# Optimization experiments

Hardware: AMD Instinct MI355X
Metric: run time of the kernel (lower is better)

## Reference

```python
import jax, jax.numpy as jnp
import numpy as np

N, F, D, H = 8192, 128, 128, 2
LEAKY_ALPHA = 0.3  # keras.layers.LeakyReLU default


def setup_inputs() -> dict:
    key = jax.random.key(0)
    ks = jax.random.split(key, 8)
    x = jax.random.normal(ks[0], (N, F), dtype=jnp.float32)
    # sparse-ish binary adjacency with self loops, stored dense (as the module does)
    adj = (jax.random.uniform(ks[1], (N, N)) < 0.01).astype(jnp.float32)
    adj = jnp.clip(adj + jnp.eye(N, dtype=jnp.float32), 0.0, 1.0)
    s = 1.0 / np.sqrt(F)
    Wmap = jax.random.normal(ks[2], (H, F, D), dtype=jnp.float32) * s
    a1_w = jax.random.normal(ks[3], (H, D), dtype=jnp.float32) * (1.0 / np.sqrt(D))
    a2_w = jax.random.normal(ks[4], (H, D), dtype=jnp.float32) * (1.0 / np.sqrt(D))
    a1_b = jnp.zeros((H,), dtype=jnp.float32)
    a2_b = jnp.zeros((H,), dtype=jnp.float32)
    kernel = jax.random.normal(ks[5], (H, F, D), dtype=jnp.float32) * s
    bias = jnp.zeros((H, N, D), dtype=jnp.float32)
    return {"x": x, "adj": adj, "Wmap": Wmap, "a1_w": a1_w, "a1_b": a1_b,
            "a2_w": a2_w, "a2_b": a2_b, "kernel": kernel, "bias": bias}


def reference(x, adj, Wmap, a1_w, a1_b, a2_w, a2_b, kernel, bias):
    # per-head Conv1D(k=1, no bias): node-wise linear map  [H, N, D]
    mapped = jnp.einsum('nf,hfd->hnd', x, Wmap)
    # per-head Conv1D(k=1) scalar scores  [H, N]
    sa1 = jnp.einsum('hnd,hd->hn', mapped, a1_w) + a1_b[:, None]
    sa2 = jnp.einsum('hnd,hd->hn', mapped, a2_w) + a2_b[:, None]
    # additive score masked multiplicatively by adjacency:  [H, N, N]
    w = adj[None, :, :] * sa1[:, :, None] + adj[None, :, :] * sa2[:, None, :]
    w = jnp.where(w >= 0, w, LEAKY_ALPHA * w)
    att = jax.nn.softmax(w, axis=-1)  # softmax over neighbors (incl. zeroed entries, as in source)
    value = jnp.einsum('nf,hfd->hnd', x, kernel)
    out = jnp.einsum('hnm,hmd->hnd', att, value) + bias  # [H, N, D]
    return out.mean(axis=0)  # attn_heads_reduction='average', linear activation
```

## Files before the change

kernel.cpp:

```cpp
#include <hip/hip_runtime.h>
#include <hip/hip_bf16.h>

#define NN 8192
#define FF 128
#define DD 128
#define HH 2
#define ALPHA 0.3f
#define MAXNNZ 1024

__global__ __launch_bounds__(256) void c_kernel(
    const float* __restrict__ Wmap, const float* __restrict__ a1w,
    const float* __restrict__ a2w, float* __restrict__ c1, float* __restrict__ c2) {
  int t = threadIdx.x;
  int h = t >> 7, f = t & 127;
  const float* wrow = Wmap + ((size_t)h * FF + f) * DD;
  const float* a1 = a1w + h * DD;
  const float* a2 = a2w + h * DD;
  float s1 = 0.f, s2 = 0.f;
  #pragma unroll 8
  for (int d = 0; d < DD; d++) {
    float w = wrow[d];
    s1 += w * a1[d];
    s2 += w * a2[d];
  }
  c1[t] = s1;
  c2[t] = s2;
}

__global__ __launch_bounds__(128) void sa_kernel(
    const float* __restrict__ x, const float* __restrict__ c1,
    const float* __restrict__ c2, const float* __restrict__ a1b,
    const float* __restrict__ a2b, float* __restrict__ sa1, float* __restrict__ sa2) {
  int n = blockIdx.x;
  int f = threadIdx.x;
  float xv = x[(size_t)n * FF + f];
  float p00 = xv * c1[f];
  float p01 = xv * c1[FF + f];
  float p10 = xv * c2[f];
  float p11 = xv * c2[FF + f];
  #pragma unroll
  for (int o = 32; o > 0; o >>= 1) {
    p00 += __shfl_down(p00, o);
    p01 += __shfl_down(p01, o);
    p10 += __shfl_down(p10, o);
    p11 += __shfl_down(p11, o);
  }
  __shared__ float part[2][4];
  int w = f >> 6;
  if ((f & 63) == 0) {
    part[w][0] = p00; part[w][1] = p01; part[w][2] = p10; part[w][3] = p11;
  }
  __syncthreads();
  if (f == 0) {
    sa1[n]      = part[0][0] + part[1][0] + a1b[0];
    sa1[NN + n] = part[0][1] + part[1][1] + a1b[1];
    sa2[n]      = part[0][2] + part[1][2] + a2b[0];
    sa2[NN + n] = part[0][3] + part[1][3] + a2b[1];
  }
}

__global__ __launch_bounds__(256) void value_gemm(
    const float* __restrict__ x, const float* __restrict__ kern,
    float* __restrict__ value) {
  int h = blockIdx.y;
  int row0 = blockIdx.x * 32;
  __shared__ float Bl[64 * 128];
  __shared__ float Al[32 * 129];
  const float4* Bg4 = (const float4*)(kern + (size_t)h * FF * DD);
  const float4* Ag4 = (const float4*)(x + (size_t)row0 * FF);
  float4* Bl4 = (float4*)Bl;
  int tid = threadIdx.x;

  #pragma unroll
  for (int q = 0; q < 4; q++) {
    int idx = q * 256 + tid;
    int r = idx >> 5, c4 = idx & 31;
    float4 g = Ag4[idx];
    Al[r * 129 + c4 * 4 + 0] = g.x;
    Al[r * 129 + c4 * 4 + 1] = g.y;
    Al[r * 129 + c4 * 4 + 2] = g.z;
    Al[r * 129 + c4 * 4 + 3] = g.w;
  }

  int cg = tid & 31;
  int rg = tid >> 5;
  float4 acc[4];
  #pragma unroll
  for (int m = 0; m < 4; m++) acc[m] = make_float4(0.f, 0.f, 0.f, 0.f);

  for (int kp = 0; kp < 2; kp++) {
    __syncthreads();
    #pragma unroll
    for (int q = 0; q < 8; q++)
      Bl4[q * 256 + tid] = Bg4[kp * 2048 + q * 256 + tid];
    __syncthreads();
    for (int k2 = 0; k2 < 64; k2++) {
      int k = kp * 64 + k2;
      float4 bv = *(const float4*)&Bl[k2 * 128 + cg * 4];
      #pragma unroll
      for (int m = 0; m < 4; m++) {
        float av = Al[(rg + m * 8) * 129 + k];
        acc[m].x += av * bv.x;
        acc[m].y += av * bv.y;
        acc[m].z += av * bv.z;
        acc[m].w += av * bv.w;
      }
    }
  }
  #pragma unroll
  for (int m = 0; m < 4; m++) {
    int r = row0 + rg + m * 8;
    *(float4*)&value[((size_t)h * NN + r) * DD + cg * 4] = acc[m];
  }
}

__global__ __launch_bounds__(128) void colsum_kernel(
    const float* __restrict__ value, float* __restrict__ colsum) {
  int h = blockIdx.y, chunk = blockIdx.x, d = threadIdx.x;
  const float* v = value + ((size_t)h * NN + (size_t)chunk * 128) * DD;
  float s = 0.f;
  #pragma unroll 4
  for (int r = 0; r < 128; r++) s += v[r * DD + d];
  atomicAdd(&colsum[h * DD + d], s);
}

__global__ __launch_bounds__(256) void gat_main(
    const float* __restrict__ adj, const float* __restrict__ sa1,
    const float* __restrict__ sa2, const float* __restrict__ value,
    const float* __restrict__ colsum, const float* __restrict__ bias,
    float* __restrict__ out) {
  int i = blockIdx.x;
  __shared__ int idxbuf[MAXNNZ];
  __shared__ float em1buf[HH][MAXNNZ];
  __shared__ int cnt;
  __shared__ float sume_sh[HH];
  __shared__ float wred[4][HH];
  __shared__ float contrib[256];
  int t = threadIdx.x;
  if (t == 0) cnt = 0;
  __syncthreads();

  const float4* arow = (const float4*)(adj + (size_t)i * NN);
  #pragma unroll
  for (int q = 0; q < 8; q++) {
    int f4 = q * 256 + t;
    float4 a = arow[f4];
    int j0 = f4 * 4;
    if (a.x != 0.f) { int p = atomicAdd(&cnt, 1); if (p < MAXNNZ) idxbuf[p] = j0; }
    if (a.y != 0.f) { int p = atomicAdd(&cnt, 1); if (p < MAXNNZ) idxbuf[p] = j0 + 1; }
    if (a.z != 0.f) { int p = atomicAdd(&cnt, 1); if (p < MAXNNZ) idxbuf[p] = j0 + 2; }
    if (a.w != 0.f) { int p = atomicAdd(&cnt, 1); if (p < MAXNNZ) idxbuf[p] = j0 + 3; }
  }
  __syncthreads();
  int count = min(cnt, MAXNNZ);

  float s10 = sa1[i];
  float s11 = sa1[NN + i];
  float l0 = 0.f, l1 = 0.f;
  for (int k = t; k < count; k += 256) {
    int j = idxbuf[k];
    float w0 = s10 + sa2[j];
    float w1 = s11 + sa2[NN + j];
    w0 = (w0 >= 0.f) ? w0 : ALPHA * w0;
    w1 = (w1 >= 0.f) ? w1 : ALPHA * w1;
    float e0 = __expf(w0) - 1.f;
    float e1 = __expf(w1) - 1.f;
    em1buf[0][k] = e0;
    em1buf[1][k] = e1;
    l0 += e0;
    l1 += e1;
  }
  #pragma unroll
  for (int o = 32; o > 0; o >>= 1) {
    l0 += __shfl_down(l0, o);
    l1 += __shfl_down(l1, o);
  }
  int wid = t >> 6;
  if ((t & 63) == 0) { wred[wid][0] = l0; wred[wid][1] = l1; }
  __syncthreads();
  if (t == 0) {
    sume_sh[0] = wred[0][0] + wred[1][0] + wred[2][0] + wred[3][0];
    sume_sh[1] = wred[0][1] + wred[1][1] + wred[2][1] + wred[3][1];
  }
  __syncthreads();

  int h = t >> 7, d = t & 127;
  const float* val = value + (size_t)h * NN * DD + d;
  const float* eb = em1buf[h];
  float acc = 0.f;
  #pragma unroll 4
  for (int k = 0; k < count; k++) {
    int j = idxbuf[k];
    acc += eb[k] * val[(size_t)j * DD];
  }
  float denom = (float)NN + sume_sh[h];
  float r = (colsum[h * DD + d] + acc) / denom +
            bias[((size_t)h * NN + i) * DD + d];
  contrib[t] = r;
  __syncthreads();
  if (t < 128) out[(size_t)i * DD + t] = 0.5f * (contrib[t] + contrib[t + 128]);
}

extern "C" void kernel_launch(void* const* d_in, const int* in_sizes, int n_in,
                              void* d_out, int out_size, void* d_ws, size_t ws_size,
                              hipStream_t stream) {
  const float* x    = (const float*)d_in[0];
  const float* adj  = (const float*)d_in[1];
  const float* Wmap = (const float*)d_in[2];
  const float* a1w  = (const float*)d_in[3];
  const float* a1b  = (const float*)d_in[4];
  const float* a2w  = (const float*)d_in[5];
  const float* a2b  = (const float*)d_in[6];
  const float* kern = (const float*)d_in[7];
  const float* bias = (const float*)d_in[8];
  float* out = (float*)d_out;
  float* ws  = (float*)d_ws;

  float* c1     = ws;
  float* c2     = ws + 256;
  float* sa1    = ws + 512;
  float* sa2    = ws + 16896;
  float* colsum = ws + 33280;
  float* value  = ws + 33536;

  hipMemsetAsync(colsum, 0, HH * DD * sizeof(float), stream);
  c_kernel<<<1, 256, 0, stream>>>(Wmap, a1w, a2w, c1, c2);
  sa_kernel<<<NN, 128, 0, stream>>>(x, c1, c2, a1b, a2b, sa1, sa2);
  value_gemm<<<dim3(NN / 32, HH), 256, 0, stream>>>(x, kern, value);
  colsum_kernel<<<dim3(NN / 128, HH), 128, 0, stream>>>(value, colsum);
  gat_main<<<NN, 256, 0, stream>>>(adj, sa1, sa2, value, colsum, bias, out);
}
```

Measured before the change: 455.5 us.

## Reassociate attention-value product to gather x rows then apply kernel GEMM

```diff
diff --git a/kernel.cpp b/kernel.cpp
--- a/kernel.cpp
+++ b/kernel.cpp
@@ -1,5 +1,4 @@
 #include <hip/hip_runtime.h>
-#include <hip/hip_bf16.h>
 
 #define NN 8192
 #define FF 128
@@ -8,23 +7,36 @@
 #define ALPHA 0.3f
 #define MAXNNZ 1024
 
-__global__ __launch_bounds__(256) void c_kernel(
+typedef float v4f __attribute__((ext_vector_type(4)));
+
+__global__ __launch_bounds__(256) void prep_kernel(
     const float* __restrict__ Wmap, const float* __restrict__ a1w,
-    const float* __restrict__ a2w, float* __restrict__ c1, float* __restrict__ c2) {
+    const float* __restrict__ a2w, const float* __restrict__ x,
+    float* __restrict__ c1, float* __restrict__ c2, float* __restrict__ xsum) {
+  int b = blockIdx.x;
   int t = threadIdx.x;
-  int h = t >> 7, f = t & 127;
-  const float* wrow = Wmap + ((size_t)h * FF + f) * DD;
-  const float* a1 = a1w + h * DD;
-  const float* a2 = a2w + h * DD;
-  float s1 = 0.f, s2 = 0.f;
-  #pragma unroll 8
-  for (int d = 0; d < DD; d++) {
-    float w = wrow[d];
-    s1 += w * a1[d];
-    s2 += w * a2[d];
-  }
-  c1[t] = s1;
-  c2[t] = s2;
+  if (b == 128) {
+    int h = t >> 7, f = t & 127;
+    const float* wrow = Wmap + ((size_t)h * FF + f) * DD;
+    const float* a1 = a1w + h * DD;
+    const float* a2 = a2w + h * DD;
+    float s1 = 0.f, s2 = 0.f;
+    #pragma unroll 8
+    for (int d = 0; d < DD; d++) {
+      float w = wrow[d];
+      s1 += w * a1[d];
+      s2 += w * a2[d];
+    }
+    c1[t] = s1;
+    c2[t] = s2;
+  } else {
+    int f = t & 127, rh = t >> 7;
+    const float* xp = x + ((size_t)(b * 64 + rh) * FF) + f;
+    float s = 0.f;
+    #pragma unroll 8
+    for (int r = 0; r < 64; r += 2) s += xp[(size_t)r * FF];
+    atomicAdd(&xsum[f], s);
+  }
 }
 
 __global__ __launch_bounds__(128) void sa_kernel(
@@ -59,92 +71,37 @@
   }
 }
 
-__global__ __launch_bounds__(256) void value_gemm(
-    const float* __restrict__ x, const float* __restrict__ kern,
-    float* __restrict__ value) {
-  int h = blockIdx.y;
-  int row0 = blockIdx.x * 32;
-  __shared__ float Bl[64 * 128];
-  __shared__ float Al[32 * 129];
-  const float4* Bg4 = (const float4*)(kern + (size_t)h * FF * DD);
-  const float4* Ag4 = (const float4*)(x + (size_t)row0 * FF);
-  float4* Bl4 = (float4*)Bl;
-  int tid = threadIdx.x;
-
-  #pragma unroll
-  for (int q = 0; q < 4; q++) {
-    int idx = q * 256 + tid;
-    int r = idx >> 5, c4 = idx & 31;
-    float4 g = Ag4[idx];
-    Al[r * 129 + c4 * 4 + 0] = g.x;
-    Al[r * 129 + c4 * 4 + 1] = g.y;
-    Al[r * 129 + c4 * 4 + 2] = g.z;
-    Al[r * 129 + c4 * 4 + 3] = g.w;
-  }
-
-  int cg = tid & 31;
-  int rg = tid >> 5;
-  float4 acc[4];
-  #pragma unroll
-  for (int m = 0; m < 4; m++) acc[m] = make_float4(0.f, 0.f, 0.f, 0.f);
-
-  for (int kp = 0; kp < 2; kp++) {
-    __syncthreads();
-    #pragma unroll
-    for (int q = 0; q < 8; q++)
-      Bl4[q * 256 + tid] = Bg4[kp * 2048 + q * 256 + tid];
-    __syncthreads();
-    for (int k2 = 0; k2 < 64; k2++) {
-      int k = kp * 64 + k2;
-      float4 bv = *(const float4*)&Bl[k2 * 128 + cg * 4];
-      #pragma unroll
-      for (int m = 0; m < 4; m++) {
-        float av = Al[(rg + m * 8) * 129 + k];
-        acc[m].x += av * bv.x;
-        acc[m].y += av * bv.y;
-        acc[m].z += av * bv.z;
-        acc[m].w += av * bv.w;
-      }
-    }
-  }
-  #pragma unroll
-  for (int m = 0; m < 4; m++) {
-    int r = row0 + rg + m * 8;
-    *(float4*)&value[((size_t)h * NN + r) * DD + cg * 4] = acc[m];
-  }
-}
-
 __global__ __launch_bounds__(128) void colsum_kernel(
-    const float* __restrict__ value, float* __restrict__ colsum) {
-  int h = blockIdx.y, chunk = blockIdx.x, d = threadIdx.x;
-  const float* v = value + ((size_t)h * NN + (size_t)chunk * 128) * DD;
+    const float* __restrict__ xsum, const float* __restrict__ kern,
+    float* __restrict__ colsum) {
+  int h = blockIdx.x, d = threadIdx.x;
+  const float* kb = kern + (size_t)h * FF * DD + d;
   float s = 0.f;
-  #pragma unroll 4
-  for (int r = 0; r < 128; r++) s += v[r * DD + d];
-  atomicAdd(&colsum[h * DD + d], s);
-}
-
-__global__ __launch_bounds__(256) void gat_main(
-    const float* __restrict__ adj, const float* __restrict__ sa1,
-    const float* __restrict__ sa2, const float* __restrict__ value,
-    const float* __restrict__ colsum, const float* __restrict__ bias,
-    float* __restrict__ out) {
+  #pragma unroll 8
+  for (int f = 0; f < FF; f++) s += xsum[f] * kb[(size_t)f * DD];
+  colsum[h * DD + d] = s;
+}
+
+__global__ __launch_bounds__(256) void gat_gather(
+    const float* __restrict__ adj, const float* __restrict__ x,
+    const float* __restrict__ sa1, const float* __restrict__ sa2,
+    float* __restrict__ gs, float* __restrict__ cinv) {
   int i = blockIdx.x;
   __shared__ int idxbuf[MAXNNZ];
   __shared__ float em1buf[HH][MAXNNZ];
   __shared__ int cnt;
+  __shared__ float wred[4][HH];
   __shared__ float sume_sh[HH];
-  __shared__ float wred[4][HH];
-  __shared__ float contrib[256];
+  __shared__ float red2[HH][FF];
   int t = threadIdx.x;
   if (t == 0) cnt = 0;
   __syncthreads();
 
-  const float4* arow = (const float4*)(adj + (size_t)i * NN);
+  const v4f* arow = (const v4f*)(adj + (size_t)i * NN);
   #pragma unroll
   for (int q = 0; q < 8; q++) {
     int f4 = q * 256 + t;
-    float4 a = arow[f4];
+    v4f a = __builtin_nontemporal_load(&arow[f4]);
     int j0 = f4 * 4;
     if (a.x != 0.f) { int p = atomicAdd(&cnt, 1); if (p < MAXNNZ) idxbuf[p] = j0; }
     if (a.y != 0.f) { int p = atomicAdd(&cnt, 1); if (p < MAXNNZ) idxbuf[p] = j0 + 1; }
@@ -184,21 +141,96 @@
   }
   __syncthreads();
 
-  int h = t >> 7, d = t & 127;
-  const float* val = value + (size_t)h * NN * DD + d;
-  const float* eb = em1buf[h];
-  float acc = 0.f;
+  int ks = t >> 7, f = t & 127;
+  float a0 = 0.f, a1 = 0.f;
+  const float* xb = x + f;
   #pragma unroll 4
-  for (int k = 0; k < count; k++) {
+  for (int k = ks; k < count; k += 2) {
     int j = idxbuf[k];
-    acc += eb[k] * val[(size_t)j * DD];
-  }
-  float denom = (float)NN + sume_sh[h];
-  float r = (colsum[h * DD + d] + acc) / denom +
-            bias[((size_t)h * NN + i) * DD + d];
-  contrib[t] = r;
-  __syncthreads();
-  if (t < 128) out[(size_t)i * DD + t] = 0.5f * (contrib[t] + contrib[t + 128]);
+    float xv = xb[(size_t)j * FF];
+    a0 += em1buf[0][k] * xv;
+    a1 += em1buf[1][k] * xv;
+  }
+  if (ks == 1) { red2[0][f] = a0; red2[1][f] = a1; }
+  __syncthreads();
+  if (ks == 0) {
+    float inv0 = 0.5f / ((float)NN + sume_sh[0]);
+    float inv1 = 0.5f / ((float)NN + sume_sh[1]);
+    float g0 = (a0 + red2[0][f]) * inv0;
+    float g1 = (a1 + red2[1][f]) * inv1;
+    gs[(size_t)i * (HH * FF) + f]      = g0;
+    gs[(size_t)i * (HH * FF) + FF + f] = g1;
+    if (f == 0) { cinv[i] = inv0; cinv[NN + i] = inv1; }
+  }
+}
+
+__global__ __launch_bounds__(256) void out_gemm(
+    const float* __restrict__ gs, const float* __restrict__ kern,
+    const float* __restrict__ cinv, const float* __restrict__ colsum,
+    const float* __restrict__ bias, float* __restrict__ out) {
+  int row0 = blockIdx.x * 32;
+  __shared__ float Bl[64 * 128];
+  __shared__ float Al[32 * 129];
+  const float4* Bg4 = (const float4*)kern;
+  const float4* Ag4 = (const float4*)(gs + (size_t)row0 * 256);
+  float4* Bl4 = (float4*)Bl;
+  int tid = threadIdx.x;
+  int cg = tid & 31;
+  int rg = tid >> 5;
+  float4 acc[4];
+  #pragma unroll
+  for (int m = 0; m < 4; m++) acc[m] = make_float4(0.f, 0.f, 0.f, 0.f);
+
+  for (int ka = 0; ka < 2; ka++) {
+    __syncthreads();
+    #pragma unroll
+    for (int q = 0; q < 4; q++) {
+      int idx = q * 256 + tid;
+      int r = idx >> 5, c4 = idx & 31;
+      float4 g = Ag4[r * 64 + ka * 32 + c4];
+      Al[r * 129 + c4 * 4 + 0] = g.x;
+      Al[r * 129 + c4 * 4 + 1] = g.y;
+      Al[r * 129 + c4 * 4 + 2] = g.z;
+      Al[r * 129 + c4 * 4 + 3] = g.w;
+    }
+    #pragma unroll
+    for (int kpi = 0; kpi < 2; kpi++) {
+      int kp = ka * 2 + kpi;
+      __syncthreads();
+      #pragma unroll
+      for (int q = 0; q < 8; q++)
+        Bl4[q * 256 + tid] = Bg4[kp * 2048 + q * 256 + tid];
+      __syncthreads();
+      for (int k2 = 0; k2 < 64; k2++) {
+        float4 bv = *(const float4*)&Bl[k2 * 128 + cg * 4];
+        #pragma unroll
+        for (int m = 0; m < 4; m++) {
+          float av = Al[(rg + m * 8) * 129 + kpi * 64 + k2];
+          acc[m].x += av * bv.x;
+          acc[m].y += av * bv.y;
+          acc[m].z += av * bv.z;
+          acc[m].w += av * bv.w;
+        }
+      }
+    }
+  }
+
+  float4 cs0 = *(const float4*)&colsum[cg * 4];
+  float4 cs1 = *(const float4*)&colsum[DD + cg * 4];
+  #pragma unroll
+  for (int m = 0; m < 4; m++) {
+    int r = row0 + rg + m * 8;
+    float ci0 = cinv[r];
+    float ci1 = cinv[NN + r];
+    float4 b0 = *(const float4*)&bias[((size_t)0 * NN + r) * DD + cg * 4];
+    float4 b1 = *(const float4*)&bias[((size_t)1 * NN + r) * DD + cg * 4];
+    float4 o;
+    o.x = acc[m].x + ci0 * cs0.x + ci1 * cs1.x + 0.5f * (b0.x + b1.x);
+    o.y = acc[m].y + ci0 * cs0.y + ci1 * cs1.y + 0.5f * (b0.y + b1.y);
+    o.z = acc[m].z + ci0 * cs0.z + ci1 * cs1.z + 0.5f * (b0.z + b1.z);
+    o.w = acc[m].w + ci0 * cs0.w + ci1 * cs1.w + 0.5f * (b0.w + b1.w);
+    *(float4*)&out[(size_t)r * DD + cg * 4] = o;
+  }
 }
 
 extern "C" void kernel_launch(void* const* d_in, const int* in_sizes, int n_in,
@@ -220,13 +252,15 @@
   float* c2     = ws + 256;
   float* sa1    = ws + 512;
   float* sa2    = ws + 16896;
-  float* colsum = ws + 33280;
-  float* value  = ws + 33536;
-
-  hipMemsetAsync(colsum, 0, HH * DD * sizeof(float), stream);
-  c_kernel<<<1, 256, 0, stream>>>(Wmap, a1w, a2w, c1, c2);
+  float* xsum   = ws + 33280;
+  float* colsum = ws + 33408;
+  float* cinv   = ws + 33664;
+  float* gs     = ws + 50048;
+
+  hipMemsetAsync(xsum, 0, FF * sizeof(float), stream);
+  prep_kernel<<<129, 256, 0, stream>>>(Wmap, a1w, a2w, x, c1, c2, xsum);
   sa_kernel<<<NN, 128, 0, stream>>>(x, c1, c2, a1b, a2b, sa1, sa2);
-  value_gemm<<<dim3(NN / 32, HH), 256, 0, stream>>>(x, kern, value);
-  colsum_kernel<<<dim3(NN / 128, HH), 128, 0, stream>>>(value, colsum);
-  gat_main<<<NN, 256, 0, stream>>>(adj, sa1, sa2, value, colsum, bias, out);
-}
+  colsum_kernel<<<HH, 128, 0, stream>>>(xsum, kern, colsum);
+  gat_gather<<<NN, 256, 0, stream>>>(adj, x, sa1, sa2, gs, cinv);
+  out_gemm<<<NN / 32, 256, 0, stream>>>(gs, kern, cinv, colsum, bias, out);
+}
```

Measured after the change: 428.6 us. 5.9% less time.
